# Kernel tuning notes

Hardware: AMD Instinct MI355X
Metric: run time of the kernel (lower is better)

Reference implementation:

```python
import jax, jax.numpy as jnp
import numpy as np

N_NODES = 50000
N_EDGES = 1_600_000
N_FEAT = 512
N_CLASSES = 16


def setup_inputs() -> dict:
    key = jax.random.key(0)
    ks = jax.random.split(key, 8)
    x = jax.random.normal(ks[0], (N_NODES, N_FEAT), dtype=jnp.float32)
    edge_index = jax.random.randint(ks[1], (2, N_EDGES), 0, N_NODES, dtype=jnp.int64)
    def glorot(k, fan_in, fan_out):
        s = jnp.sqrt(6.0 / (fan_in + fan_out)).astype(jnp.float32)
        return jax.random.uniform(k, (fan_in, fan_out), jnp.float32, -s, s)
    W1 = glorot(ks[2], N_FEAT, 256)
    W2 = glorot(ks[3], 256, 32)
    W3 = glorot(ks[4], 32, N_CLASSES)
    b1 = jnp.zeros((256,), jnp.float32)
    b2 = jnp.zeros((32,), jnp.float32)
    b3 = jnp.zeros((N_CLASSES,), jnp.float32)
    return {"x": x, "edge_index": edge_index, "W1": W1, "b1": b1,
            "W2": W2, "b2": b2, "W3": W3, "b3": b3}


def _gcn_norm(edge_index, num_nodes):
    # add self loops, compute symmetric normalization D^-1/2 (A+I) D^-1/2
    loop = jnp.arange(num_nodes, dtype=edge_index.dtype)
    src = jnp.concatenate([edge_index[0], loop])  # message source (x_j)
    dst = jnp.concatenate([edge_index[1], loop])  # aggregation target
    ones = jnp.ones(dst.shape[0], jnp.float32)
    deg = jax.ops.segment_sum(ones, dst, num_segments=num_nodes)
    dis = jnp.where(deg > 0, jax.lax.rsqrt(deg), 0.0)  # deg_inv_sqrt
    norm = dis[src] * dis[dst]  # [E+N]
    return src, dst, norm


def _gcn_conv(x, src, dst, norm, W, b, num_nodes):
    h = x @ W  # [N, out] dense transform first (as PyG does)
    msg = h[src] * norm[:, None]  # gather + scale, [E+N, out]
    out = jax.ops.segment_sum(msg, dst, num_segments=num_nodes)
    return out + b


def reference(x, edge_index, W1, b1, W2, b2, W3, b3):
    n = x.shape[0]
    src, dst, norm = _gcn_norm(edge_index, n)
    h = jax.nn.relu(_gcn_conv(x, src, dst, norm, W1, b1, n))
    h = jax.nn.relu(_gcn_conv(h, src, dst, norm, W2, b2, n))
    return _gcn_conv(h, src, dst, norm, W3, b3, n)
```

## Files before the change

### kernel.cpp

```cpp
#include <hip/hip_runtime.h>

#define N_NODES 50000
#define N_EDGES 1600000

typedef __bf16 bf16x8 __attribute__((ext_vector_type(8)));
typedef float f32x4 __attribute__((ext_vector_type(4)));
typedef _Float16 h8v __attribute__((ext_vector_type(8)));
typedef _Float16 h4v __attribute__((ext_vector_type(4)));


__global__ __launch_bounds__(256) void k_deg(const int* __restrict__ dst, int* __restrict__ deg) {
  int e = blockIdx.x * 256 + threadIdx.x;
  if (e < N_EDGES) atomicAdd(&deg[dst[e]], 1);
}

__global__ __launch_bounds__(256) void k_dis(const int* __restrict__ deg, float* __restrict__ dis) {
  int v = blockIdx.x * 256 + threadIdx.x;
  if (v < N_NODES) dis[v] = 1.0f / sqrtf((float)(deg[v] + 1));
}

__global__ __launch_bounds__(1024) void k_scanA(const int* __restrict__ deg, int* __restrict__ incl,
                                                int* __restrict__ bsum) {
  __shared__ int sm[1024];
  int b = blockIdx.x, t = threadIdx.x;
  int idx = b * 1024 + t;
  int v = (idx < N_NODES) ? deg[idx] : 0;
  sm[t] = v;
  __syncthreads();
  for (int off = 1; off < 1024; off <<= 1) {
    int u = (t >= off) ? sm[t - off] : 0;
    __syncthreads();
    sm[t] += u;
    __syncthreads();
  }
  incl[idx] = sm[t];
  if (t == 1023) bsum[b] = sm[1023];
}

__global__ __launch_bounds__(64) void k_scanB(const int* __restrict__ bsum, int* __restrict__ bofs) {
  int t = threadIdx.x;
  int v = (t < 49) ? bsum[t] : 0;
  for (int off = 1; off < 64; off <<= 1) {
    int u = __shfl_up(v, off);
    if (t >= off) v += u;
  }
  int ex = __shfl_up(v, 1);
  if (t == 0) ex = 0;
  if (t < 50) bofs[t] = ex;
}

__global__ __launch_bounds__(1024) void k_scanC(const int* __restrict__ deg, const int* __restrict__ incl,
                                                const int* __restrict__ bofs, int* __restrict__ rp) {
  int b = blockIdx.x, t = threadIdx.x;
  int idx = b * 1024 + t;
  if (idx < N_NODES) rp[idx] = bofs[b] + incl[idx] - deg[idx];
  if (idx == N_NODES) rp[idx] = bofs[49];
}

__global__ __launch_bounds__(256) void k_fill(const int* __restrict__ src, const int* __restrict__ dst,
                                              const float* __restrict__ dis, const int* __restrict__ rp,
                                              int* __restrict__ cursor, int* __restrict__ col,
                                              float* __restrict__ wgt) {
  int e = blockIdx.x * 256 + threadIdx.x;
  if (e >= N_EDGES) return;
  int s = src[e], d = dst[e];
  int p = rp[d] + atomicAdd(&cursor[d], 1);
  col[p] = s;
  wgt[p] = dis[s] * dis[d];
}


__global__ __launch_bounds__(256) void k_wsplit(const float* __restrict__ W1, ushort* __restrict__ Wt) {
  int idx = blockIdx.x * 256 + threadIdx.x;
  if (idx >= 512 * 256) return;
  int k = idx >> 8, n = idx & 255;
  float v = W1[idx];
  unsigned u = __float_as_uint(v);
  float fhi = __uint_as_float(u & 0xFFFF0000u);
  float r = v - fhi;
  Wt[n * 1024 + k] = (ushort)(u >> 16);
  Wt[n * 1024 + 512 + k] = (ushort)(__float_as_uint(r) >> 16);
}


__device__ __forceinline__ void gload16(const void* g, void* l) {
  __builtin_amdgcn_global_load_lds((const __attribute__((address_space(1))) void*)g,
                                   (__attribute__((address_space(3))) void*)l, 16, 0, 0);
}

__device__ __forceinline__ void cvt8(const float4& f0, const float4& f1, uint4& hi, uint4& lo) {
  float a[8] = {f0.x, f0.y, f0.z, f0.w, f1.x, f1.y, f1.z, f1.w};
  unsigned h[4], lw[4];
#pragma unroll
  for (int i = 0; i < 4; ++i) {
    unsigned u0 = __float_as_uint(a[2 * i]);
    float r0 = a[2 * i] - __uint_as_float(u0 & 0xFFFF0000u);
    float r1 = a[2 * i + 1] - __uint_as_float(__float_as_uint(a[2 * i + 1]) & 0xFFFF0000u);
    h[i] = (u0 >> 16) | (__float_as_uint(a[2 * i + 1]) & 0xFFFF0000u);
    lw[i] = (__float_as_uint(r0) >> 16) | (__float_as_uint(r1) & 0xFFFF0000u);
  }
  hi = make_uint4(h[0], h[1], h[2], h[3]);
  lo = make_uint4(lw[0], lw[1], lw[2], lw[3]);
}

__global__ __launch_bounds__(256) void k_gemm1_mfma(const float* __restrict__ X,
                                                    const ushort* __restrict__ Wt,
                                                    _Float16* __restrict__ C, int M) {
  __shared__ __align__(16) ushort Ahi[2][4096], Alo[2][4096], Bhi[2][4096], Blo[2][4096];
  const int t = threadIdx.x;
  const int lane = t & 63;
  const int w = t >> 6;
  const int wm = w >> 1, wn = w & 1;
  const int bm = blockIdx.x * 128;
  const int bn = blockIdx.y * 128;

  f32x4 acc[4][4] = {};

  const int o0 = t * 16;
  const int r0 = o0 >> 6;
  const int kk0 = (t & 3) * 8;
  int gr0 = bm + r0; if (gr0 >= M) gr0 = M - 1;
  int gr1 = bm + r0 + 64; if (gr1 >= M) gr1 = M - 1;
  const float* xrow0 = X + (size_t)gr0 * 512 + kk0;
  const float* xrow1 = X + (size_t)gr1 * 512 + kk0;

  const int ob = w * 1024 + lane * 16;
  const int n0 = ob >> 6, k0 = (lane & 3) * 8;
  const int n1 = n0 + 64;
  const int wl = w * 1024;
  const size_t wt0 = (size_t)(bn + n0) * 1024 + k0;
  const size_t wt1 = (size_t)(bn + n1) * 1024 + k0;

  gload16(Wt + wt0, (char*)Bhi[0] + wl);
  gload16(Wt + wt1, (char*)Bhi[0] + wl + 4096);
  gload16(Wt + wt0 + 512, (char*)Blo[0] + wl);
  gload16(Wt + wt1 + 512, (char*)Blo[0] + wl + 4096);
  float4 f0 = *(const float4*)(xrow0);
  float4 f1 = *(const float4*)(xrow0 + 4);
  float4 f2 = *(const float4*)(xrow1);
  float4 f3 = *(const float4*)(xrow1 + 4);
  {
    uint4 h0, l0, h1, l1;
    cvt8(f0, f1, h0, l0);
    cvt8(f2, f3, h1, l1);
    *(uint4*)((char*)Ahi[0] + o0) = h0;
    *(uint4*)((char*)Alo[0] + o0) = l0;
    *(uint4*)((char*)Ahi[0] + o0 + 4096) = h1;
    *(uint4*)((char*)Alo[0] + o0 + 4096) = l1;
  }
  __syncthreads();

  for (int tt = 0; tt < 16; ++tt) {
    const int cur = tt & 1, nxt = cur ^ 1;
    if (tt < 15) {
      const int ktn = (tt + 1) * 32;
      gload16(Wt + wt0 + ktn, (char*)Bhi[nxt] + wl);
      gload16(Wt + wt1 + ktn, (char*)Bhi[nxt] + wl + 4096);
      gload16(Wt + wt0 + 512 + ktn, (char*)Blo[nxt] + wl);
      gload16(Wt + wt1 + 512 + ktn, (char*)Blo[nxt] + wl + 4096);
      f0 = *(const float4*)(xrow0 + ktn);
      f1 = *(const float4*)(xrow0 + ktn + 4);
      f2 = *(const float4*)(xrow1 + ktn);
      f3 = *(const float4*)(xrow1 + ktn + 4);
    }
    const int kb = (lane >> 4) * 16;
    bf16x8 ah[4], al[4], bh[4], bl[4];
#pragma unroll
    for (int i = 0; i < 4; ++i) {
      int ra = (wm * 64 + i * 16 + (lane & 15)) * 64 + kb;
      ah[i] = *(const bf16x8*)((char*)Ahi[cur] + ra);
      al[i] = *(const bf16x8*)((char*)Alo[cur] + ra);
      int rb = (wn * 64 + i * 16 + (lane & 15)) * 64 + kb;
      bh[i] = *(const bf16x8*)((char*)Bhi[cur] + rb);
      bl[i] = *(const bf16x8*)((char*)Blo[cur] + rb);
    }
#pragma unroll
    for (int i = 0; i < 4; ++i)
#pragma unroll
      for (int j = 0; j < 4; ++j) {
        acc[i][j] = __builtin_amdgcn_mfma_f32_16x16x32_bf16(ah[i], bh[j], acc[i][j], 0, 0, 0);
        acc[i][j] = __builtin_amdgcn_mfma_f32_16x16x32_bf16(ah[i], bl[j], acc[i][j], 0, 0, 0);
        acc[i][j] = __builtin_amdgcn_mfma_f32_16x16x32_bf16(al[i], bh[j], acc[i][j], 0, 0, 0);
      }
    if (tt < 15) {
      uint4 h0, l0, h1, l1;
      cvt8(f0, f1, h0, l0);
      cvt8(f2, f3, h1, l1);
      *(uint4*)((char*)Ahi[nxt] + o0) = h0;
      *(uint4*)((char*)Alo[nxt] + o0) = l0;
      *(uint4*)((char*)Ahi[nxt] + o0 + 4096) = h1;
      *(uint4*)((char*)Alo[nxt] + o0 + 4096) = l1;
    }
    __syncthreads();
  }

#pragma unroll
  for (int i = 0; i < 4; ++i) {
#pragma unroll
    for (int j = 0; j < 4; ++j) {
#pragma unroll
      for (int r = 0; r < 4; ++r) {
        int grow = bm + wm * 64 + i * 16 + (lane >> 4) * 4 + r;
        int gcol = bn + wn * 64 + j * 16 + (lane & 15);
        if (grow < M) C[(size_t)grow * 256 + gcol] = (_Float16)acc[i][j][r];
      }
    }
  }
}


__global__ __launch_bounds__(256) void k_gemm2h(const _Float16* __restrict__ A, const float* __restrict__ B,
                                                _Float16* __restrict__ C, int M) {
  __shared__ float As[32][128];
  __shared__ float Bs[32][32];
  const int t = threadIdx.x;
  const int bm = blockIdx.x * 128;
  const int ty = t >> 3, tx = t & 7;
  float acc[4][4] = {};
  for (int kt = 0; kt < 256; kt += 32) {
#pragma unroll
    for (int jj = 0; jj < 2; ++jj) {
      int slot = t + jj * 256;
      int r = slot >> 2, c8 = slot & 3;
      int row = bm + r; if (row >= M) row = M - 1;
      h8v val = *(const h8v*)(A + (size_t)row * 256 + kt + c8 * 8);
#pragma unroll
      for (int q = 0; q < 8; ++q) As[c8 * 8 + q][r] = (float)val[q];
    }
    {
      int r = t >> 3, c4 = t & 7;
      *(float4*)&Bs[r][c4 * 4] = *(const float4*)(B + (size_t)(kt + r) * 32 + c4 * 4);
    }
    __syncthreads();
#pragma unroll
    for (int k = 0; k < 32; ++k) {
      float a[4], b[4];
      *(float4*)a = *(const float4*)&As[k][ty * 4];
      *(float4*)b = *(const float4*)&Bs[k][tx * 4];
#pragma unroll
      for (int i = 0; i < 4; ++i)
#pragma unroll
        for (int j = 0; j < 4; ++j) acc[i][j] += a[i] * b[j];
    }
    __syncthreads();
  }
#pragma unroll
  for (int i = 0; i < 4; ++i) {
    int row = bm + ty * 4 + i;
    if (row < M) {
#pragma unroll
      for (int j = 0; j < 4; ++j) C[(size_t)row * 32 + tx * 4 + j] = (_Float16)acc[i][j];
    }
  }
}


__global__ __launch_bounds__(256) void k_agg256h(const _Float16* __restrict__ h, const int* __restrict__ col,
                                                 const float* __restrict__ wgt, const int* __restrict__ rp,
                                                 const float* __restrict__ dis, const float* __restrict__ bias,
                                                 _Float16* __restrict__ out) {
  int v = (blockIdx.x * 256 + threadIdx.x) >> 6;
  int lane = threadIdx.x & 63;
  if (v >= N_NODES) return;
  int slot = lane >> 5;
  int l5 = lane & 31;
  float d = dis[v];
  float sw = d * d;
  float acc[8];
  h8v self = *(const h8v*)(h + (size_t)v * 256 + l5 * 8);
#pragma unroll
  for (int j = 0; j < 8; ++j) acc[j] = (slot == 0) ? sw * (float)self[j] : 0.f;
  int s = rp[v], e = rp[v + 1];
  for (int i = s; i < e; i += 8) {
    int i0 = i + slot, i1 = i + 2 + slot, i2 = i + 4 + slot, i3 = i + 6 + slot;
    int c0 = (i0 < e) ? col[i0] : v;  float w0 = (i0 < e) ? wgt[i0] : 0.f;
    int c1 = (i1 < e) ? col[i1] : v;  float w1 = (i1 < e) ? wgt[i1] : 0.f;
    int c2 = (i2 < e) ? col[i2] : v;  float w2 = (i2 < e) ? wgt[i2] : 0.f;
    int c3 = (i3 < e) ? col[i3] : v;  float w3 = (i3 < e) ? wgt[i3] : 0.f;
    h8v x0 = *(const h8v*)(h + (size_t)c0 * 256 + l5 * 8);
    h8v x1 = *(const h8v*)(h + (size_t)c1 * 256 + l5 * 8);
    h8v x2 = *(const h8v*)(h + (size_t)c2 * 256 + l5 * 8);
    h8v x3 = *(const h8v*)(h + (size_t)c3 * 256 + l5 * 8);
#pragma unroll
    for (int j = 0; j < 8; ++j)
      acc[j] += w0 * (float)x0[j] + w1 * (float)x1[j] + w2 * (float)x2[j] + w3 * (float)x3[j];
  }
#pragma unroll
  for (int j = 0; j < 8; ++j) acc[j] += __shfl_xor(acc[j], 32);
  if (slot == 0) {
    float4 b0 = *(const float4*)(bias + l5 * 8);
    float4 b1 = *(const float4*)(bias + l5 * 8 + 4);
    float bb[8] = {b0.x, b0.y, b0.z, b0.w, b1.x, b1.y, b1.z, b1.w};
    h8v o;
#pragma unroll
    for (int j = 0; j < 8; ++j) o[j] = (_Float16)fmaxf(acc[j] + bb[j], 0.f);
    *(h8v*)(out + (size_t)v * 256 + l5 * 8) = o;
  }
}

__global__ __launch_bounds__(256) void k_agg32w3(const _Float16* __restrict__ h, const int* __restrict__ col,
                                                 const float* __restrict__ wgt, const int* __restrict__ rp,
                                                 const float* __restrict__ dis, const float* __restrict__ b2,
                                                 const float* __restrict__ W3, _Float16* __restrict__ out) {
  __shared__ float W3s[512];
  __shared__ float rowbuf[4][32];
  int t = threadIdx.x;
  for (int i = t; i < 512; i += 256) W3s[i] = W3[i];
  __syncthreads();
  int v = (blockIdx.x * 256 + t) >> 6;
  int lane = t & 63;
  int wv = t >> 6;
  int slot = lane >> 3, f4 = lane & 7;
  float d = dis[v];
  float sw = d * d;
  float acc[4];
  h4v self = *(const h4v*)(h + (size_t)v * 32 + f4 * 4);
#pragma unroll
  for (int j = 0; j < 4; ++j) acc[j] = (slot == 0) ? sw * (float)self[j] : 0.f;
  int s = rp[v], e = rp[v + 1];
  for (int i = s; i < e; i += 16) {
    int i0 = i + slot, i1 = i + 8 + slot;
    int c0 = (i0 < e) ? col[i0] : v;  float w0 = (i0 < e) ? wgt[i0] : 0.f;
    int c1 = (i1 < e) ? col[i1] : v;  float w1 = (i1 < e) ? wgt[i1] : 0.f;
    h4v x0 = *(const h4v*)(h + (size_t)c0 * 32 + f4 * 4);
    h4v x1 = *(const h4v*)(h + (size_t)c1 * 32 + f4 * 4);
#pragma unroll
    for (int j = 0; j < 4; ++j) acc[j] += w0 * (float)x0[j] + w1 * (float)x1[j];
  }
#pragma unroll
  for (int off = 8; off < 64; off <<= 1) {
#pragma unroll
    for (int j = 0; j < 4; ++j) acc[j] += __shfl_xor(acc[j], off);
  }
  float4 bb = *(const float4*)(b2 + f4 * 4);
  float g0 = fmaxf(acc[0] + bb.x, 0.f), g1 = fmaxf(acc[1] + bb.y, 0.f);
  float g2 = fmaxf(acc[2] + bb.z, 0.f), g3 = fmaxf(acc[3] + bb.w, 0.f);
  if (lane < 8) *(float4*)&rowbuf[wv][f4 * 4] = make_float4(g0, g1, g2, g3);
  int j = lane & 15;
  float o = 0.f;
#pragma unroll
  for (int k4 = 0; k4 < 8; ++k4) {
    float4 rr = *(const float4*)&rowbuf[wv][k4 * 4];
    o += rr.x * W3s[(k4 * 4 + 0) * 16 + j] + rr.y * W3s[(k4 * 4 + 1) * 16 + j]
       + rr.z * W3s[(k4 * 4 + 2) * 16 + j] + rr.w * W3s[(k4 * 4 + 3) * 16 + j];
  }
  if (lane < 16) out[(size_t)v * 16 + j] = (_Float16)o;
}

__global__ __launch_bounds__(256) void k_agg16(const _Float16* __restrict__ h, const int* __restrict__ col,
                                               const float* __restrict__ wgt, const int* __restrict__ rp,
                                               const float* __restrict__ dis, const float* __restrict__ bias,
                                               float* __restrict__ out) {
  constexpr int LPE = 4, NS = 16;
  int v = (blockIdx.x * 256 + threadIdx.x) >> 6;
  int lane = threadIdx.x & 63;
  if (v >= N_NODES) return;
  int slot = lane / LPE;
  int f4 = lane % LPE;
  float d = dis[v];
  float sw = d * d;
  float acc[4] = {0.f, 0.f, 0.f, 0.f};
  h4v self = *(const h4v*)(h + (size_t)v * 16 + f4 * 4);
  if (slot == 0) {
#pragma unroll
    for (int j = 0; j < 4; ++j) acc[j] = sw * (float)self[j];
  }
  int s = rp[v], e = rp[v + 1];
  for (int i = s + slot; i < e; i += NS) {
    int c = col[i];
    float wt = wgt[i];
    h4v x = *(const h4v*)(h + (size_t)c * 16 + f4 * 4);
#pragma unroll
    for (int j = 0; j < 4; ++j) acc[j] += wt * (float)x[j];
  }
#pragma unroll
  for (int off = LPE; off < 64; off <<= 1) {
#pragma unroll
    for (int j = 0; j < 4; ++j) acc[j] += __shfl_xor(acc[j], off);
  }
  if (slot == 0) {
    float4 b = *(const float4*)(bias + f4 * 4);
    acc[0] += b.x; acc[1] += b.y; acc[2] += b.z; acc[3] += b.w;
    *(float4*)(out + (size_t)v * 16 + f4 * 4) = make_float4(acc[0], acc[1], acc[2], acc[3]);
  }
}


extern "C" void kernel_launch(void* const* d_in, const int* in_sizes, int n_in,
                              void* d_out, int out_size, void* d_ws, size_t ws_size,
                              hipStream_t stream) {
  const float* x  = (const float*)d_in[0];
  const int*   ei = (const int*)d_in[1];
  const float* W1 = (const float*)d_in[2];
  const float* b1 = (const float*)d_in[3];
  const float* W2 = (const float*)d_in[4];
  const float* b2 = (const float*)d_in[5];
  const float* W3 = (const float*)d_in[6];
  const float* b3 = (const float*)d_in[7];
  float* out = (float*)d_out;

  _Float16* h1h = (_Float16*)d_ws;
  _Float16* g1h = h1h + (size_t)N_NODES * 256;
  _Float16* h2h = g1h + (size_t)N_NODES * 256;
  _Float16* h3h = h2h + (size_t)N_NODES * 32;
  ushort*   Wt  = (ushort*)(h3h + (size_t)N_NODES * 16);
  int*      deg = (int*)(Wt + 256 * 1024);
  int*      cur = deg + N_NODES;
  float*    dis = (float*)(cur + N_NODES);
  int*      rp  = (int*)(dis + N_NODES);
  int*      incl = rp + (N_NODES + 1);
  int*      bsum = incl + 49 * 1024;
  int*      bofs = bsum + 64;
  int*      col = bofs + 64;
  float*    wgt = (float*)(col + N_EDGES);

  const int* src = ei;
  const int* dst = ei + N_EDGES;

  hipMemsetAsync(deg, 0, 2 * (size_t)N_NODES * sizeof(int), stream);
  k_deg<<<(N_EDGES + 255) / 256, 256, 0, stream>>>(dst, deg);
  k_dis<<<(N_NODES + 255) / 256, 256, 0, stream>>>(deg, dis);
  k_scanA<<<49, 1024, 0, stream>>>(deg, incl, bsum);
  k_scanB<<<1, 64, 0, stream>>>(bsum, bofs);
  k_scanC<<<49, 1024, 0, stream>>>(deg, incl, bofs, rp);
  k_fill<<<(N_EDGES + 255) / 256, 256, 0, stream>>>(src, dst, dis, rp, cur, col, wgt);
  k_wsplit<<<512, 256, 0, stream>>>(W1, Wt);

  dim3 gg1((N_NODES + 127) / 128, 2);
  k_gemm1_mfma<<<gg1, 256, 0, stream>>>(x, Wt, h1h, N_NODES);
  k_agg256h<<<(N_NODES + 3) / 4, 256, 0, stream>>>(h1h, col, wgt, rp, dis, b1, g1h);

  k_gemm2h<<<(N_NODES + 127) / 128, 256, 0, stream>>>(g1h, W2, h2h, N_NODES);

  k_agg32w3<<<(N_NODES + 3) / 4, 256, 0, stream>>>(h2h, col, wgt, rp, dis, b2, W3, h3h);

  k_agg16<<<(N_NODES + 3) / 4, 256, 0, stream>>>(h3h, col, wgt, rp, dis, b3, out);
}
```

Measured before the change: 447.9 us.

## Drop per-edge weight array; recompute norm from dis in aggregation kernels

```diff
diff --git a/kernel.cpp b/kernel.cpp
--- a/kernel.cpp
+++ b/kernel.cpp
@@ -58,15 +58,12 @@
 }
 
 __global__ __launch_bounds__(256) void k_fill(const int* __restrict__ src, const int* __restrict__ dst,
-                                              const float* __restrict__ dis, const int* __restrict__ rp,
-                                              int* __restrict__ cursor, int* __restrict__ col,
-                                              float* __restrict__ wgt) {
+                                              int* __restrict__ cursor, int* __restrict__ col) {
   int e = blockIdx.x * 256 + threadIdx.x;
   if (e >= N_EDGES) return;
   int s = src[e], d = dst[e];
-  int p = rp[d] + atomicAdd(&cursor[d], 1);
+  int p = atomicAdd(&cursor[d], 1);
   col[p] = s;
-  wgt[p] = dis[s] * dis[d];
 }
 
 
@@ -256,7 +253,7 @@
 
 
 __global__ __launch_bounds__(256) void k_agg256h(const _Float16* __restrict__ h, const int* __restrict__ col,
-                                                 const float* __restrict__ wgt, const int* __restrict__ rp,
+                                                 const int* __restrict__ rp,
                                                  const float* __restrict__ dis, const float* __restrict__ bias,
                                                  _Float16* __restrict__ out) {
   int v = (blockIdx.x * 256 + threadIdx.x) >> 6;
@@ -264,8 +261,8 @@
   if (v >= N_NODES) return;
   int slot = lane >> 5;
   int l5 = lane & 31;
-  float d = dis[v];
-  float sw = d * d;
+  float dv = dis[v];
+  float sw = dv * dv;
   float acc[8];
   h8v self = *(const h8v*)(h + (size_t)v * 256 + l5 * 8);
 #pragma unroll
@@ -273,10 +270,10 @@
   int s = rp[v], e = rp[v + 1];
   for (int i = s; i < e; i += 8) {
     int i0 = i + slot, i1 = i + 2 + slot, i2 = i + 4 + slot, i3 = i + 6 + slot;
-    int c0 = (i0 < e) ? col[i0] : v;  float w0 = (i0 < e) ? wgt[i0] : 0.f;
-    int c1 = (i1 < e) ? col[i1] : v;  float w1 = (i1 < e) ? wgt[i1] : 0.f;
-    int c2 = (i2 < e) ? col[i2] : v;  float w2 = (i2 < e) ? wgt[i2] : 0.f;
-    int c3 = (i3 < e) ? col[i3] : v;  float w3 = (i3 < e) ? wgt[i3] : 0.f;
+    int c0 = (i0 < e) ? col[i0] : v;  float w0 = (i0 < e) ? dis[c0] * dv : 0.f;
+    int c1 = (i1 < e) ? col[i1] : v;  float w1 = (i1 < e) ? dis[c1] * dv : 0.f;
+    int c2 = (i2 < e) ? col[i2] : v;  float w2 = (i2 < e) ? dis[c2] * dv : 0.f;
+    int c3 = (i3 < e) ? col[i3] : v;  float w3 = (i3 < e) ? dis[c3] * dv : 0.f;
     h8v x0 = *(const h8v*)(h + (size_t)c0 * 256 + l5 * 8);
     h8v x1 = *(const h8v*)(h + (size_t)c1 * 256 + l5 * 8);
     h8v x2 = *(const h8v*)(h + (size_t)c2 * 256 + l5 * 8);
@@ -299,7 +296,7 @@
 }
 
 __global__ __launch_bounds__(256) void k_agg32w3(const _Float16* __restrict__ h, const int* __restrict__ col,
-                                                 const float* __restrict__ wgt, const int* __restrict__ rp,
+                                                 const int* __restrict__ rp,
                                                  const float* __restrict__ dis, const float* __restrict__ b2,
                                                  const float* __restrict__ W3, _Float16* __restrict__ out) {
   __shared__ float W3s[512];
@@ -311,8 +308,8 @@
   int lane = t & 63;
   int wv = t >> 6;
   int slot = lane >> 3, f4 = lane & 7;
-  float d = dis[v];
-  float sw = d * d;
+  float dv = dis[v];
+  float sw = dv * dv;
   float acc[4];
   h4v self = *(const h4v*)(h + (size_t)v * 32 + f4 * 4);
 #pragma unroll
@@ -320,8 +317,8 @@
   int s = rp[v], e = rp[v + 1];
   for (int i = s; i < e; i += 16) {
     int i0 = i + slot, i1 = i + 8 + slot;
-    int c0 = (i0 < e) ? col[i0] : v;  float w0 = (i0 < e) ? wgt[i0] : 0.f;
-    int c1 = (i1 < e) ? col[i1] : v;  float w1 = (i1 < e) ? wgt[i1] : 0.f;
+    int c0 = (i0 < e) ? col[i0] : v;  float w0 = (i0 < e) ? dis[c0] * dv : 0.f;
+    int c1 = (i1 < e) ? col[i1] : v;  float w1 = (i1 < e) ? dis[c1] * dv : 0.f;
     h4v x0 = *(const h4v*)(h + (size_t)c0 * 32 + f4 * 4);
     h4v x1 = *(const h4v*)(h + (size_t)c1 * 32 + f4 * 4);
 #pragma unroll
@@ -348,7 +345,7 @@
 }
 
 __global__ __launch_bounds__(256) void k_agg16(const _Float16* __restrict__ h, const int* __restrict__ col,
-                                               const float* __restrict__ wgt, const int* __restrict__ rp,
+                                               const int* __restrict__ rp,
                                                const float* __restrict__ dis, const float* __restrict__ bias,
                                                float* __restrict__ out) {
   constexpr int LPE = 4, NS = 16;
@@ -357,8 +354,8 @@
   if (v >= N_NODES) return;
   int slot = lane / LPE;
   int f4 = lane % LPE;
-  float d = dis[v];
-  float sw = d * d;
+  float dv = dis[v];
+  float sw = dv * dv;
   float acc[4] = {0.f, 0.f, 0.f, 0.f};
   h4v self = *(const h4v*)(h + (size_t)v * 16 + f4 * 4);
   if (slot == 0) {
@@ -368,7 +365,7 @@
   int s = rp[v], e = rp[v + 1];
   for (int i = s + slot; i < e; i += NS) {
     int c = col[i];
-    float wt = wgt[i];
+    float wt = dis[c] * dv;
     h4v x = *(const h4v*)(h + (size_t)c * 16 + f4 * 4);
 #pragma unroll
     for (int j = 0; j < 4; ++j) acc[j] += wt * (float)x[j];
@@ -412,27 +409,27 @@
   int*      bsum = incl + 49 * 1024;
   int*      bofs = bsum + 64;
   int*      col = bofs + 64;
-  float*    wgt = (float*)(col + N_EDGES);
 
   const int* src = ei;
   const int* dst = ei + N_EDGES;
 
-  hipMemsetAsync(deg, 0, 2 * (size_t)N_NODES * sizeof(int), stream);
+  hipMemsetAsync(deg, 0, (size_t)N_NODES * sizeof(int), stream);
   k_deg<<<(N_EDGES + 255) / 256, 256, 0, stream>>>(dst, deg);
   k_dis<<<(N_NODES + 255) / 256, 256, 0, stream>>>(deg, dis);
   k_scanA<<<49, 1024, 0, stream>>>(deg, incl, bsum);
   k_scanB<<<1, 64, 0, stream>>>(bsum, bofs);
   k_scanC<<<49, 1024, 0, stream>>>(deg, incl, bofs, rp);
-  k_fill<<<(N_EDGES + 255) / 256, 256, 0, stream>>>(src, dst, dis, rp, cur, col, wgt);
+  hipMemcpyAsync(cur, rp, (size_t)N_NODES * sizeof(int), hipMemcpyDeviceToDevice, stream);
+  k_fill<<<(N_EDGES + 255) / 256, 256, 0, stream>>>(src, dst, cur, col);
   k_wsplit<<<512, 256, 0, stream>>>(W1, Wt);
 
   dim3 gg1((N_NODES + 127) / 128, 2);
   k_gemm1_mfma<<<gg1, 256, 0, stream>>>(x, Wt, h1h, N_NODES);
-  k_agg256h<<<(N_NODES + 3) / 4, 256, 0, stream>>>(h1h, col, wgt, rp, dis, b1, g1h);
+  k_agg256h<<<(N_NODES + 3) / 4, 256, 0, stream>>>(h1h, col, rp, dis, b1, g1h);
 
   k_gemm2h<<<(N_NODES + 127) / 128, 256, 0, stream>>>(g1h, W2, h2h, N_NODES);
 
-  k_agg32w3<<<(N_NODES + 3) / 4, 256, 0, stream>>>(h2h, col, wgt, rp, dis, b2, W3, h3h);
-
-  k_agg16<<<(N_NODES + 3) / 4, 256, 0, stream>>>(h3h, col, wgt, rp, dis, b3, out);
-}
+  k_agg32w3<<<(N_NODES + 3) / 4, 256, 0, stream>>>(h2h, col, rp, dis, b2, W3, h3h);
+
+  k_agg16<<<(N_NODES + 3) / 4, 256, 0, stream>>>(h3h, col, rp, dis, b3, out);
+}
```

Result: slower. 497.7 us (+11.1%).

## Build CSR with two-pass bucketed fill instead of per-node atomic scatter

Applied to the files above, without the earlier changes.

```diff
diff --git a/kernel.cpp b/kernel.cpp
--- a/kernel.cpp
+++ b/kernel.cpp
@@ -2,6 +2,7 @@
 
 #define N_NODES 50000
 #define N_EDGES 1600000
+#define NBUCK 3125
 
 typedef __bf16 bf16x8 __attribute__((ext_vector_type(8)));
 typedef float f32x4 __attribute__((ext_vector_type(4)));
@@ -57,16 +58,39 @@
   if (idx == N_NODES) rp[idx] = bofs[49];
 }
 
-__global__ __launch_bounds__(256) void k_fill(const int* __restrict__ src, const int* __restrict__ dst,
-                                              const float* __restrict__ dis, const int* __restrict__ rp,
-                                              int* __restrict__ cursor, int* __restrict__ col,
-                                              float* __restrict__ wgt) {
+__global__ __launch_bounds__(256) void k_binit(const int* __restrict__ rp, int* __restrict__ bcur) {
+  int b = blockIdx.x * 256 + threadIdx.x;
+  if (b < NBUCK) bcur[b] = rp[b * 16];
+}
+
+__global__ __launch_bounds__(256) void k_pass1(const int* __restrict__ src, const int* __restrict__ dst,
+                                               int* __restrict__ bcur, int* __restrict__ tmp) {
   int e = blockIdx.x * 256 + threadIdx.x;
   if (e >= N_EDGES) return;
   int s = src[e], d = dst[e];
-  int p = rp[d] + atomicAdd(&cursor[d], 1);
-  col[p] = s;
-  wgt[p] = dis[s] * dis[d];
+  int p = atomicAdd(&bcur[d >> 4], 1);
+  tmp[p] = (s << 4) | (d & 15);
+}
+
+__global__ __launch_bounds__(256) void k_pass2(const int* __restrict__ rp, const int* __restrict__ tmp,
+                                               const float* __restrict__ dis,
+                                               int* __restrict__ col, float* __restrict__ wgt) {
+  __shared__ int curs[4][16];
+  int t = threadIdx.x;
+  int wv = t >> 6, lane = t & 63;
+  int bucket = blockIdx.x * 4 + wv;
+  int b16 = bucket * 16;
+  if (bucket < NBUCK && lane < 16) curs[wv][lane] = rp[b16 + lane];
+  __syncthreads();
+  if (bucket >= NBUCK) return;
+  int base = rp[b16], endp = rp[b16 + 16];
+  for (int i = base + lane; i < endp; i += 64) {
+    int rec = tmp[i];
+    int s = rec >> 4, dl = rec & 15;
+    int p = atomicAdd(&curs[wv][dl], 1);
+    col[p] = s;
+    wgt[p] = dis[s] * dis[b16 + dl];
+  }
 }
 
 
@@ -264,8 +288,8 @@
   if (v >= N_NODES) return;
   int slot = lane >> 5;
   int l5 = lane & 31;
-  float d = dis[v];
-  float sw = d * d;
+  float dv = dis[v];
+  float sw = dv * dv;
   float acc[8];
   h8v self = *(const h8v*)(h + (size_t)v * 256 + l5 * 8);
 #pragma unroll
@@ -311,8 +335,8 @@
   int lane = t & 63;
   int wv = t >> 6;
   int slot = lane >> 3, f4 = lane & 7;
-  float d = dis[v];
-  float sw = d * d;
+  float dv = dis[v];
+  float sw = dv * dv;
   float acc[4];
   h4v self = *(const h4v*)(h + (size_t)v * 32 + f4 * 4);
 #pragma unroll
@@ -357,8 +381,8 @@
   if (v >= N_NODES) return;
   int slot = lane / LPE;
   int f4 = lane % LPE;
-  float d = dis[v];
-  float sw = d * d;
+  float dv = dis[v];
+  float sw = dv * dv;
   float acc[4] = {0.f, 0.f, 0.f, 0.f};
   h4v self = *(const h4v*)(h + (size_t)v * 16 + f4 * 4);
   if (slot == 0) {
@@ -405,25 +429,28 @@
   _Float16* h3h = h2h + (size_t)N_NODES * 32;
   ushort*   Wt  = (ushort*)(h3h + (size_t)N_NODES * 16);
   int*      deg = (int*)(Wt + 256 * 1024);
-  int*      cur = deg + N_NODES;
-  float*    dis = (float*)(cur + N_NODES);
+  float*    dis = (float*)(deg + N_NODES);
   int*      rp  = (int*)(dis + N_NODES);
   int*      incl = rp + (N_NODES + 1);
   int*      bsum = incl + 49 * 1024;
   int*      bofs = bsum + 64;
-  int*      col = bofs + 64;
+  int*      bcur = bofs + 64;
+  int*      tmp = bcur + NBUCK + 3;
+  int*      col = tmp + N_EDGES;
   float*    wgt = (float*)(col + N_EDGES);
 
   const int* src = ei;
   const int* dst = ei + N_EDGES;
 
-  hipMemsetAsync(deg, 0, 2 * (size_t)N_NODES * sizeof(int), stream);
+  hipMemsetAsync(deg, 0, (size_t)N_NODES * sizeof(int), stream);
   k_deg<<<(N_EDGES + 255) / 256, 256, 0, stream>>>(dst, deg);
   k_dis<<<(N_NODES + 255) / 256, 256, 0, stream>>>(deg, dis);
   k_scanA<<<49, 1024, 0, stream>>>(deg, incl, bsum);
   k_scanB<<<1, 64, 0, stream>>>(bsum, bofs);
   k_scanC<<<49, 1024, 0, stream>>>(deg, incl, bofs, rp);
-  k_fill<<<(N_EDGES + 255) / 256, 256, 0, stream>>>(src, dst, dis, rp, cur, col, wgt);
+  k_binit<<<(NBUCK + 255) / 256, 256, 0, stream>>>(rp, bcur);
+  k_pass1<<<(N_EDGES + 255) / 256, 256, 0, stream>>>(src, dst, bcur, tmp);
+  k_pass2<<<(NBUCK + 3) / 4, 256, 0, stream>>>(rp, tmp, dis, col, wgt);
   k_wsplit<<<512, 256, 0, stream>>>(W1, Wt);
 
   dim3 gg1((N_NODES + 127) / 128, 2);
```

Result: slower. 506.2 us (+13.0%).
